# Performance work log

Measured on AMD Instinct MI355X. Metric: run time of the kernel, lower is better.

Reference implementation:

```python
import jax, jax.numpy as jnp
import numpy as np

N_DOF = 7
WIDTH = 1024
BATCH = 8192
EPS = 1e-5
LSIZE = N_DOF * (N_DOF + 1) // 2   # diag (n) + strictly-lower ((n^2-n)/2)


def _tri_idx(n):
    # order matches LowTri: offset -i chunks, within-chunk j -> entry (j+i, j)
    r, c = [], []
    for i in range(n):
        for j in range(n - i):
            r.append(j + i)
            c.append(j)
    return np.array(r, np.int32), np.array(c, np.int32)

_R, _C = _tri_idx(N_DOF)


def setup_inputs() -> dict:
    key = jax.random.key(0)
    ks = jax.random.split(key, 9)

    def glorot(k, shape):
        std = (2.0 / (shape[0] + shape[1])) ** 0.5
        return (jax.random.normal(k, shape, jnp.float32) * std).astype(jnp.float32)

    lower = LSIZE - N_DOF
    b0 = 0.1
    return {
        "state": jax.random.normal(ks[0], (BATCH, N_DOF), jnp.float32),
        "velocity": jax.random.normal(ks[1], (BATCH, N_DOF), jnp.float32),
        "acceleration": jax.random.normal(ks[2], (BATCH, N_DOF), jnp.float32),
        "W_in": glorot(ks[3], (N_DOF, WIDTH)), "b_in": jnp.full((WIDTH,), b0, jnp.float32),
        "W_h": glorot(ks[4], (WIDTH, WIDTH)), "b_h": jnp.full((WIDTH,), b0, jnp.float32),
        "W_g": glorot(ks[5], (WIDTH, 1)), "b_g": jnp.full((1,), b0, jnp.float32),
        "W_ld": glorot(ks[6], (WIDTH, N_DOF)), "b_ld": jnp.full((N_DOF,), b0, jnp.float32),
        "W_lo": glorot(ks[7], (WIDTH, lower)), "b_lo": jnp.full((lower,), b0, jnp.float32),
    }


def _layer(x, der, W, b, act):
    # a: [B, out]; der: [B, in, n_dof] -> [B, out, n_dof]
    a = x @ W + b
    if act == "relu":
        y = jax.nn.relu(a)
        gp = (a > 0).astype(a.dtype)
    else:  # linear
        y = a
        gp = jnp.ones_like(a)
    # diag(g'(a)) @ W^T @ prev_der  ==  g'(a)[:, :, None] * (W^T @ prev_der)
    new_der = gp[:, :, None] * jnp.einsum("io,bid->bod", W, der)
    return y, new_der


def _forward(state, velocity, acceleration,
             W_in, b_in, W_h, b_h, W_g, b_g, W_ld, b_ld, W_lo, b_lo):
    B = state.shape[0]
    eye = jnp.broadcast_to(jnp.eye(N_DOF, dtype=state.dtype), (B, N_DOF, N_DOF))

    y1, d1 = _layer(state, eye, W_in, b_in, "relu")
    y2, d2 = _layer(y1, d1, W_h, b_h, "relu")
    y3, d3 = _layer(y2, d2, W_h, b_h, "relu")   # original reuses hidden_layer1 twice

    V, derV = _layer(y3, d3, W_g, b_g, "linear")       # derV: [B, 1, n_dof]
    l_diag, der_ld = _layer(y3, d3, W_ld, b_ld, "relu")
    l_low, der_lo = _layer(y3, d3, W_lo, b_lo, "linear")

    l = jnp.concatenate([l_diag, l_low], axis=1)          # [B, LSIZE]
    der_l = jnp.concatenate([der_ld, der_lo], axis=1)     # [B, LSIZE, n_dof]

    def lowtri(v):   # [B, LSIZE] -> [B, n, n]
        return jnp.zeros((B, N_DOF, N_DOF), v.dtype).at[:, _R, _C].set(v)

    def lowtri3d(v):  # [B, n_dof, LSIZE] -> [B, n_dof, n, n]
        return jnp.zeros((B, N_DOF, N_DOF, N_DOF), v.dtype).at[:, :, _R, _C].set(v)

    L = lowtri(l)
    LT = jnp.swapaxes(L, 1, 2)
    M = L @ LT + EPS * jnp.eye(N_DOF, dtype=L.dtype)

    dldt = jnp.einsum("bld,bd->bl", der_l, velocity)
    dLdt = lowtri(dldt)
    dMdt = L @ jnp.swapaxes(dLdt, 1, 2) + dLdt @ LT

    dLdq = lowtri3d(jnp.swapaxes(der_l, 1, 2))            # [B, n_dof, n, n]
    dMdq = dLdq @ LT[:, None] + L[:, None] @ jnp.swapaxes(dLdq, 2, 3)

    dMdt_dq = jnp.einsum("bij,bj->bi", dMdt, velocity)
    quad_dq = jnp.einsum("bi,bkij,bj->bk", velocity, dMdq, velocity)
    C = dMdt_dq - 0.5 * quad_dq
    G = derV[:, 0, :]                                      # squeeze [B,1,n_dof]
    Mddq = jnp.einsum("bij,bj->bi", M, acceleration)
    tau_pred = Mddq + C + G
    return tau_pred, M, C, G


def reference(state, velocity, acceleration,
              W_in, b_in, W_h, b_h, W_g, b_g, W_ld, b_ld, W_lo, b_lo):
    return _forward(state, velocity, acceleration,
                    W_in, b_in, W_h, b_h, W_g, b_g, W_ld, b_ld, W_lo, b_lo)
```

## Files before the change

### kernel.cpp

```cpp
#include <hip/hip_runtime.h>
#include <hip/hip_bf16.h>
#include <hip/hip_fp16.h>

#define WIDTH 1024
#define BATCH 8192

typedef __attribute__((ext_vector_type(8))) short short8;
typedef __attribute__((ext_vector_type(8))) _Float16 half8;
typedef __attribute__((ext_vector_type(4))) float floatx4;

typedef __attribute__((address_space(1))) void gvoid;
typedef __attribute__((address_space(3))) void lvoid;

__device__ __forceinline__ void async_copy16(const void* g, void* l) {
    __builtin_amdgcn_global_load_lds((gvoid*)g, (lvoid*)l, 16, 0, 0);
}

__device__ __forceinline__ void split_store(float v, __hip_bfloat16* hi, __hip_bfloat16* lo, long idx) {
    __hip_bfloat16 h = __float2bfloat16(v);
    hi[idx] = h;
    lo[idx] = __float2bfloat16(v - __bfloat162float(h));
}

__device__ __forceinline__ floatx4 mfma16(short8 a, short8 b, floatx4 c) {
    return __builtin_amdgcn_mfma_f32_16x16x32_f16(
        __builtin_bit_cast(half8, a), __builtin_bit_cast(half8, b), c, 0, 0, 0);
}
__device__ __forceinline__ floatx4 mfmabf(short8 a, short8 b, floatx4 c) {
    return __builtin_amdgcn_mfma_f32_16x16x32_bf16(a, b, c, 0, 0, 0);
}

template<int N> __device__ __forceinline__ void waitv() {
    if constexpr (N == 0)      asm volatile("s_waitcnt vmcnt(0)" ::: "memory");
    else if constexpr (N == 1) asm volatile("s_waitcnt vmcnt(1)" ::: "memory");
    else if constexpr (N == 3) asm volatile("s_waitcnt vmcnt(3)" ::: "memory");
    else if constexpr (N == 4) asm volatile("s_waitcnt vmcnt(4)" ::: "memory");
    else if constexpr (N == 6) asm volatile("s_waitcnt vmcnt(6)" ::: "memory");
    else if constexpr (N == 7) asm volatile("s_waitcnt vmcnt(7)" ::: "memory");
    else if constexpr (N == 8) asm volatile("s_waitcnt vmcnt(8)" ::: "memory");
    else if constexpr (N == 9) asm volatile("s_waitcnt vmcnt(9)" ::: "memory");
}

__device__ __forceinline__ int swz_col(int s) {
    return ((s & 3) ^ ((s >> 3) & 3)) << 3;
}

__device__ __forceinline__ void xcd_map(int idx, int nm, int& bm, int& bn) {
    if ((nm & 7) == 0) {
        bm = (idx & 7) | ((idx >> 5) << 3);
        bn = (idx >> 3) & 3;
    } else {
        bm = idx >> 2;
        bn = idx & 3;
    }
}

__global__ __launch_bounds__(256) void transpose_k(
    const float* __restrict__ W,
    __hip_bfloat16* __restrict__ Wthb, __hip_bfloat16* __restrict__ Wtlb,
    __half* __restrict__ Wtf)
{
    __shared__ float t[32][33];
    const int tx = threadIdx.x & 31, ty = threadIdx.x >> 5;
    const int bx = blockIdx.x << 5, by = blockIdx.y << 5;
#pragma unroll
    for (int r = 0; r < 32; r += 8)
        t[ty + r][tx] = W[(long)(by + ty + r) * WIDTH + bx + tx];
    __syncthreads();
#pragma unroll
    for (int r = 0; r < 32; r += 8) {
        const float v = t[tx][ty + r];
        const long idx = (long)(bx + ty + r) * WIDTH + by + tx;
        split_store(v, Wthb, Wtlb, idx);
        Wtf[idx] = __float2half(v);
    }
}

__global__ __launch_bounds__(256) void buildwcat_k(
    const float* __restrict__ W_ld, const float* __restrict__ W_lo,
    const float* __restrict__ W_g,
    __hip_bfloat16* __restrict__ Wchb, __hip_bfloat16* __restrict__ Wclb,
    __half* __restrict__ Wcf)
{
    const int idx = blockIdx.x * 256 + threadIdx.x;
    const int n = idx >> 10, k = idx & 1023;
    float v = 0.f;
    if (n < 7)       v = W_ld[k * 7 + n];
    else if (n < 28) v = W_lo[k * 21 + (n - 7)];
    else if (n == 28) v = W_g[k];
    split_store(v, Wchb, Wclb, idx);
    Wcf[idx] = __float2half(v);
}

__global__ __launch_bounds__(256) void prep_k(
    const float* __restrict__ state,
    const float* __restrict__ W_in,
    const float* __restrict__ b_in,
    __hip_bfloat16* __restrict__ Y1h, __hip_bfloat16* __restrict__ Y1l,
    __half* __restrict__ D1f)
{
    const int b = blockIdx.x;
    const int j0 = threadIdx.x * 4;
    float s[7];
#pragma unroll
    for (int d = 0; d < 7; ++d) s[d] = state[b * 7 + d];
    float a[4];
#pragma unroll
    for (int q = 0; q < 4; ++q) a[q] = b_in[j0 + q];
    float w[7][4];
#pragma unroll
    for (int d = 0; d < 7; ++d)
#pragma unroll
        for (int q = 0; q < 4; ++q) {
            w[d][q] = W_in[d * WIDTH + j0 + q];
            a[q] += s[d] * w[d][q];
        }
    bool gp[4];
#pragma unroll
    for (int q = 0; q < 4; ++q) {
        gp[q] = a[q] > 0.f;
        split_store(gp[q] ? a[q] : 0.f, Y1h, Y1l, (long)b * WIDTH + j0 + q);
    }
    union { unsigned long long u64; unsigned short h[4]; } pk;
#pragma unroll
    for (int d = 0; d < 7; ++d) {
#pragma unroll
        for (int q = 0; q < 4; ++q) {
            __half v = __float2half(gp[q] ? w[d][q] : 0.f);
            pk.h[q] = *reinterpret_cast<unsigned short*>(&v);
        }
        *reinterpret_cast<unsigned long long*>(&D1f[((long)b * 7 + d) * WIDTH + j0]) = pk.u64;
    }
}


__device__ __forceinline__ void st128(const short* src, short* region, int tid, int kbase) {
    async_copy16(src + (long)(tid >> 2) * WIDTH + kbase + swz_col(tid),
                 region + ((tid & 0x1C0) << 3));
}
__device__ __forceinline__ void st256(const short* src, short* region, int tid, int kbase) {
#pragma unroll
    for (int j = 0; j < 2; ++j) {
        const int idx = tid + (j << 9);
        async_copy16(src + (long)(idx >> 2) * WIDTH + kbase + swz_col(idx),
                     region + (((tid & 0x1C0) + (j << 9)) << 3));
    }
}

template<int W0, int W1, int W2, int IS>
__device__ __forceinline__ void y8_triple(
    short* buf, short* nbuf,
    const short* pAh, const short* pAl, const short* pBh, const short* pBl,
    int t, int tid, int wm, int wn, int r, int kqs, floatx4 (&acc)[4][4])
{
    short8 fah[4], fbh[4];
#pragma unroll
    for (int i = 0; i < 4; ++i)
        fah[i] = *reinterpret_cast<const short8*>(&buf[(wm * 64 + i * 16 + r) * 32 + kqs]);
#pragma unroll
    for (int j = 0; j < 4; ++j)
        fbh[j] = *reinterpret_cast<const short8*>(&buf[8192 + (wn * 64 + j * 16 + r) * 32 + kqs]);
    if (IS >= 1) st128(pAl, nbuf + 4096, tid, (t + 1) * 32);
    __builtin_amdgcn_s_barrier();
    asm volatile("s_waitcnt lgkmcnt(0)");
    __builtin_amdgcn_sched_barrier(0);
    __builtin_amdgcn_s_setprio(1);
#pragma unroll
    for (int i = 0; i < 4; ++i)
#pragma unroll
        for (int j = 0; j < 4; ++j)
            acc[i][j] = mfmabf(fah[i], fbh[j], acc[i][j]);
    __builtin_amdgcn_s_setprio(0);
    waitv<W0>();
    __builtin_amdgcn_s_barrier();
    short8 fbl[4];
#pragma unroll
    for (int j = 0; j < 4; ++j)
        fbl[j] = *reinterpret_cast<const short8*>(&buf[16384 + (wn * 64 + j * 16 + r) * 32 + kqs]);
    if (IS >= 2) { st128(pAh, buf, tid, (t + 2) * 32); st256(pBh, buf + 8192, tid, (t + 2) * 32); }
    __builtin_amdgcn_s_barrier();
    asm volatile("s_waitcnt lgkmcnt(0)");
    __builtin_amdgcn_sched_barrier(0);
    __builtin_amdgcn_s_setprio(1);
#pragma unroll
    for (int i = 0; i < 4; ++i)
#pragma unroll
        for (int j = 0; j < 4; ++j)
            acc[i][j] = mfmabf(fah[i], fbl[j], acc[i][j]);
    __builtin_amdgcn_s_setprio(0);
    waitv<W1>();
    __builtin_amdgcn_s_barrier();
    short8 fal[4];
#pragma unroll
    for (int i = 0; i < 4; ++i)
        fal[i] = *reinterpret_cast<const short8*>(&buf[4096 + (wm * 64 + i * 16 + r) * 32 + kqs]);
    if (IS >= 2) st256(pBl, buf + 16384, tid, (t + 2) * 32);
    __builtin_amdgcn_s_barrier();
    asm volatile("s_waitcnt lgkmcnt(0)");
    __builtin_amdgcn_sched_barrier(0);
    __builtin_amdgcn_s_setprio(1);
#pragma unroll
    for (int i = 0; i < 4; ++i)
#pragma unroll
        for (int j = 0; j < 4; ++j)
            acc[i][j] = mfmabf(fal[i], fbh[j], acc[i][j]);
    __builtin_amdgcn_s_setprio(0);
    waitv<W2>();
    __builtin_amdgcn_s_barrier();
}

__device__ __forceinline__ void y8_gemm_body(
    short* SM,
    int bm, int bn, int tid,
    const __hip_bfloat16* Ah_, const __hip_bfloat16* Al_,
    const __hip_bfloat16* Bh_, const __hip_bfloat16* Bl_,
    const float* bias,
    __hip_bfloat16* outh, __hip_bfloat16* outl)
{
    const int lane = tid & 63, wv = tid >> 6;
    const int wm = wv >> 2, wn = wv & 3;
    const int r = lane & 15, r4 = (lane >> 4) << 2;
    const int kqs = (((lane >> 4) ^ ((r >> 1) & 3)) << 3);
    const short* pAh = (const short*)Ah_ + (long)bm * 128 * WIDTH;
    const short* pAl = (const short*)Al_ + (long)bm * 128 * WIDTH;
    const short* pBh = (const short*)Bh_ + (long)bn * 256 * WIDTH;
    const short* pBl = (const short*)Bl_ + (long)bn * 256 * WIDTH;

    floatx4 acc[4][4] = {};

    st128(pAh, SM + 0,     tid, 0);
    st256(pBh, SM + 8192,  tid, 0);
    st256(pBl, SM + 16384, tid, 0);
    st128(pAl, SM + 4096,  tid, 0);
    st128(pAh, SM + 24576 + 0,     tid, 32);
    st256(pBh, SM + 24576 + 8192,  tid, 32);
    st256(pBl, SM + 24576 + 16384, tid, 32);
    waitv<8>();
    __builtin_amdgcn_s_barrier();

    for (int t2 = 0; t2 < 15; ++t2) {
        y8_triple<7, 9, 8, 2>(SM,         SM + 24576, pAh, pAl, pBh, pBl, 2 * t2,     tid, wm, wn, r, kqs, acc);
        y8_triple<7, 9, 8, 2>(SM + 24576, SM,         pAh, pAl, pBh, pBl, 2 * t2 + 1, tid, wm, wn, r, kqs, acc);
    }
    y8_triple<7, 6, 3, 1>(SM,         SM + 24576, pAh, pAl, pBh, pBl, 30, tid, wm, wn, r, kqs, acc);
    y8_triple<1, 0, 0, 0>(SM + 24576, SM,         pAh, pAl, pBh, pBl, 31, tid, wm, wn, r, kqs, acc);

#pragma unroll
    for (int i = 0; i < 4; ++i)
#pragma unroll
        for (int j = 0; j < 4; ++j) {
            const int col = bn * 256 + wn * 64 + j * 16 + r;
#pragma unroll
            for (int rr = 0; rr < 4; ++rr) {
                const int row = bm * 128 + wm * 64 + i * 16 + r4 + rr;
                float v = acc[i][j][rr] + bias[col];
                v = v > 0.f ? v : 0.f;
                split_store(v, outh, outl, (long)row * WIDTH + col);
            }
        }
}

__global__ __launch_bounds__(512, 2) void gemm_y8(
    const __hip_bfloat16* __restrict__ Ah, const __hip_bfloat16* __restrict__ Al,
    const __hip_bfloat16* __restrict__ Bh, const __hip_bfloat16* __restrict__ Bl,
    const float* __restrict__ bias,
    __hip_bfloat16* __restrict__ outh, __hip_bfloat16* __restrict__ outl,
    int ny)
{
    __shared__ __align__(16) short SM[49152];
    int bm, bn;
    xcd_map(blockIdx.x, ny, bm, bn);
    y8_gemm_body(SM, bm, bn, threadIdx.x, Ah, Al, Bh, Bl, bias, outh, outl);
}

__device__ __forceinline__ void stage_chunk_d2(
    short* SMbase, const short* __restrict__ A, const short* __restrict__ B,
    int tau, int c, int tid)
{
    const short* src = (c & 1) ? B : A;
    const int kbase = (tau << 6) + ((c >> 1) << 5);
    short* region = SMbase + ((tau & 1) << 15) + (c << 13);
    const int wvb = tid & 0x1C0;
#pragma unroll
    for (int j = 0; j < 2; ++j) {
        const int idx = tid + (j << 9);
        async_copy16(src + (long)(idx >> 2) * WIDTH + kbase + swz_col(idx),
                     region + ((long)(wvb + (j << 9)) << 3));
    }
}

__device__ __forceinline__ void d_gemm_256(
    short* SM, const short* Abase, const short* Bbase, int tid,
    int wm, int wn, int r, int kqs, floatx4 (&acc)[8][4])
{
    stage_chunk_d2(SM, Abase, Bbase, 0, 0, tid);
    stage_chunk_d2(SM, Abase, Bbase, 0, 1, tid);
    stage_chunk_d2(SM, Abase, Bbase, 0, 2, tid);
    stage_chunk_d2(SM, Abase, Bbase, 0, 3, tid);
    stage_chunk_d2(SM, Abase, Bbase, 1, 0, tid);
    stage_chunk_d2(SM, Abase, Bbase, 1, 1, tid);
    waitv<8>();
    __builtin_amdgcn_s_barrier();

    short8 af[8], bf[4];
#pragma unroll 2
    for (int t = 0; t < 16; ++t) {
        short* buf = SM + ((t & 1) << 15);
#pragma unroll
        for (int ks = 0; ks < 2; ++ks) {
            const short* Ab = buf + (ks ? 2 : 0) * 8192;
            const short* Bb = buf + (ks ? 3 : 1) * 8192;

#pragma unroll
            for (int i = 0; i < 4; ++i)
                af[i] = *reinterpret_cast<const short8*>(&Ab[(wm * 128 + i * 16 + r) * 32 + kqs]);
#pragma unroll
            for (int j = 0; j < 4; ++j)
                bf[j] = *reinterpret_cast<const short8*>(&Bb[(wn * 64 + j * 16 + r) * 32 + kqs]);
            if (ks == 0) { if (t + 1 < 16) stage_chunk_d2(SM, Abase, Bbase, t + 1, 2, tid); }
            else         { if (t + 2 < 16) stage_chunk_d2(SM, Abase, Bbase, t + 2, 0, tid); }
            __builtin_amdgcn_s_barrier();
            asm volatile("s_waitcnt lgkmcnt(0)");
            __builtin_amdgcn_sched_barrier(0);
            __builtin_amdgcn_s_setprio(1);
#pragma unroll
            for (int i = 0; i < 4; ++i)
#pragma unroll
                for (int j = 0; j < 4; ++j)
                    acc[i][j] = mfma16(af[i], bf[j], acc[i][j]);
            __builtin_amdgcn_s_setprio(0);
            __builtin_amdgcn_s_barrier();

#pragma unroll
            for (int i = 0; i < 4; ++i)
                af[4 + i] = *reinterpret_cast<const short8*>(&Ab[(wm * 128 + (4 + i) * 16 + r) * 32 + kqs]);
            if (ks == 0) { if (t + 1 < 16) stage_chunk_d2(SM, Abase, Bbase, t + 1, 3, tid); }
            else         { if (t + 2 < 16) stage_chunk_d2(SM, Abase, Bbase, t + 2, 1, tid); }
            __builtin_amdgcn_s_barrier();
            asm volatile("s_waitcnt lgkmcnt(0)");
            __builtin_amdgcn_sched_barrier(0);
            __builtin_amdgcn_s_setprio(1);
#pragma unroll
            for (int i = 0; i < 4; ++i)
#pragma unroll
                for (int j = 0; j < 4; ++j)
                    acc[4 + i][j] = mfma16(af[4 + i], bf[j], acc[4 + i][j]);
            __builtin_amdgcn_s_setprio(0);
            if (ks == 0) {
                if (t < 15) waitv<8>(); else waitv<0>();
            } else {
                if (t < 14) waitv<8>(); else if (t == 14) waitv<4>();
            }
            __builtin_amdgcn_s_barrier();
        }
    }
}

__global__ __launch_bounds__(512, 2) void d2y3_8p(
    const __half* __restrict__ D1,
    const __half* __restrict__ Wtf,
    const __hip_bfloat16* __restrict__ Wthb, const __hip_bfloat16* __restrict__ Wtlb,
    const __hip_bfloat16* __restrict__ Y2h, const __hip_bfloat16* __restrict__ Y2l,
    const float* __restrict__ bias,
    __half* __restrict__ D2out,
    __hip_bfloat16* __restrict__ Y3h, __hip_bfloat16* __restrict__ Y3l,
    int ny128, int nd2)
{
    __shared__ __align__(16) short SM[65536];
    const int tid = threadIdx.x;

    if ((int)blockIdx.x < ny128 * 4) {
        int bm, bn;
        xcd_map(blockIdx.x, ny128, bm, bn);
        y8_gemm_body(SM, bm, bn, tid, Y2h, Y2l, Wthb, Wtlb, bias, Y3h, Y3l);
        return;
    }

    const int lane = tid & 63, wv = tid >> 6;
    const int wm = wv >> 2, wn = wv & 3;
    const int r = lane & 15, r4 = (lane >> 4) << 2;
    const int kqs = (((lane >> 4) ^ ((r >> 1) & 3)) << 3);

    int bm, bn;
    xcd_map(blockIdx.x - ny128 * 4, nd2, bm, bn);

    floatx4 acc[8][4] = {};
    d_gemm_256(SM, (const short*)D1 + (long)bm * 256 * WIDTH,
               (const short*)Wtf + (long)bn * 256 * WIDTH, tid, wm, wn, r, kqs, acc);

#pragma unroll
    for (int i = 0; i < 8; ++i)
#pragma unroll
        for (int j = 0; j < 4; ++j) {
            const int col = bn * 256 + wn * 64 + j * 16 + r;
#pragma unroll
            for (int rr = 0; rr < 4; ++rr) {
                const int row = bm * 256 + wm * 128 + i * 16 + r4 + rr;
                float v = acc[i][j][rr];
                const unsigned brow = (unsigned)row / 7u;
                if (!(__bfloat162float(Y2h[(long)brow * WIDTH + col]) > 0.f)) v = 0.f;
                D2out[(long)row * WIDTH + col] = __float2half(v);
            }
        }
}

__device__ __forceinline__ void heady_half(
    short* SMh, int bm, int tl,
    const __hip_bfloat16* __restrict__ Y3h, const __hip_bfloat16* __restrict__ Y3l,
    const __hip_bfloat16* __restrict__ Wch, const __hip_bfloat16* __restrict__ Wcl,
    float* __restrict__ PY)
{
    short* Ash = SMh;          short* Asl = SMh + 4096;
    short* Bsh = SMh + 8192;   short* Bsl = SMh + 9216;
    const int lane = tl & 63;
    const int wv = tl >> 6;
    const int r = lane & 15, r4 = (lane >> 4) << 2;
    const int kqs = (((lane >> 4) ^ ((r >> 1) & 3)) << 3);
    const int srow = tl >> 2, scol = (tl & 3) << 3;
    const int swc = (((tl & 3) ^ ((srow >> 1) & 3)) << 3);
    const long half = 64l * WIDTH;
    const short* pAh = (const short*)Y3h + (long)(bm * 128 + srow) * WIDTH + swc;
    const short* pAl = (const short*)Y3l + (long)(bm * 128 + srow) * WIDTH + swc;
    const long boff = (long)srow * WIDTH + scol;
    const short* pBh = (const short*)Wch;  const short* pBl = (const short*)Wcl;

    floatx4 acc[2][2] = {};
    for (int kt = 0; kt < WIDTH; kt += 32) {
        short8 gbh, gbl;
        if (tl < 128) {
            gbh = *reinterpret_cast<const short8*>(pBh + boff + kt);
            gbl = *reinterpret_cast<const short8*>(pBl + boff + kt);
        }
        __syncthreads();
        async_copy16(pAh + kt,        Ash + wv * 512);
        async_copy16(pAh + half + kt, Ash + 2048 + wv * 512);
        async_copy16(pAl + kt,        Asl + wv * 512);
        async_copy16(pAl + half + kt, Asl + 2048 + wv * 512);
        if (tl < 128) {
            *reinterpret_cast<short8*>(&Bsh[srow * 32 + swc]) = gbh;
            *reinterpret_cast<short8*>(&Bsl[srow * 32 + swc]) = gbl;
        }
        __syncthreads();
        short8 afh[2], afl[2], bfh[2], bfl[2];
#pragma unroll
        for (int i = 0; i < 2; ++i) {
            const int ar = (wv * 32 + i * 16 + r) * 32 + kqs;
            afh[i] = *reinterpret_cast<const short8*>(&Ash[ar]);
            afl[i] = *reinterpret_cast<const short8*>(&Asl[ar]);
        }
#pragma unroll
        for (int j = 0; j < 2; ++j) {
            const int br = (j * 16 + r) * 32 + kqs;
            bfh[j] = *reinterpret_cast<const short8*>(&Bsh[br]);
            bfl[j] = *reinterpret_cast<const short8*>(&Bsl[br]);
        }
#pragma unroll
        for (int i = 0; i < 2; ++i)
#pragma unroll
            for (int j = 0; j < 2; ++j) {
                acc[i][j] = mfmabf(afh[i], bfh[j], acc[i][j]);
                acc[i][j] = mfmabf(afh[i], bfl[j], acc[i][j]);
                acc[i][j] = mfmabf(afl[i], bfh[j], acc[i][j]);
            }
    }
#pragma unroll
    for (int i = 0; i < 2; ++i)
#pragma unroll
        for (int j = 0; j < 2; ++j)
#pragma unroll
            for (int rr = 0; rr < 4; ++rr) {
                const int row = bm * 128 + wv * 32 + i * 16 + r4 + rr;
                PY[(long)row * 32 + j * 16 + r] = acc[i][j][rr];
            }
}

__global__ __launch_bounds__(512, 2) void d3pd_8p(
    const __half* __restrict__ D2,
    const __half* __restrict__ Wtf,
    const __hip_bfloat16* __restrict__ Y3h, const __hip_bfloat16* __restrict__ Y3l,
    const __half* __restrict__ Wcf,
    const __hip_bfloat16* __restrict__ Wchb, const __hip_bfloat16* __restrict__ Wclb,
    float* __restrict__ PDpart, float* __restrict__ PY,
    int nd2, int Mrows)
{
    __shared__ __align__(16) short SM[65536];
    const int tid = threadIdx.x;

    if ((int)blockIdx.x >= nd2 * 4) {
        const int hd = (blockIdx.x - nd2 * 4) * 2 + (tid >> 8);
        heady_half(SM + (tid >> 8) * 10240, hd, tid & 255, Y3h, Y3l, Wchb, Wclb, PY);
        return;
    }

    const int lane = tid & 63, wv = tid >> 6;
    const int wm = wv >> 2, wn = wv & 3;
    const int r = lane & 15, kq = (lane >> 4) << 3, r4 = (lane >> 4) << 2;
    const int kqs = (((lane >> 4) ^ ((r >> 1) & 3)) << 3);
    int bm, bn;
    xcd_map(blockIdx.x, nd2, bm, bn);

    floatx4 acc[8][4] = {};
    d_gemm_256(SM, (const short*)D2 + (long)bm * 256 * WIDTH,
               (const short*)Wtf + (long)bn * 256 * WIDTH, tid, wm, wn, r, kqs, acc);

    short* T   = SM;
    short* WcH = SM + 34816;

    floatx4 accp[2][2] = {};
#pragma unroll
    for (int h = 0; h < 2; ++h) {
        __syncthreads();
        if ((wn >> 1) == h) {
#pragma unroll
            for (int i = 0; i < 8; ++i)
#pragma unroll
                for (int j = 0; j < 4; ++j) {
                    const int ct = (wn & 1) * 64 + j * 16 + r;
                    const int colg = bn * 256 + h * 128 + ct;
#pragma unroll
                    for (int rr = 0; rr < 4; ++rr) {
                        const int rowl = wm * 128 + i * 16 + r4 + rr;
                        const int rowg = bm * 256 + rowl;
                        float v = acc[i][j][rr];
                        const unsigned brow = (unsigned)rowg / 7u;
                        if (!(__bfloat162float(Y3h[(long)brow * WIDTH + colg]) > 0.f)) v = 0.f;
                        __half hb = __float2half(v);
                        T[rowl * 136 + ct] = *reinterpret_cast<short*>(&hb);
                    }
                }
        }
        {
            const int n = tid >> 4, k8 = (tid & 15) * 8;
            const short* wh = (const short*)Wcf;
            *reinterpret_cast<short8*>(&WcH[n * 136 + k8]) =
                *reinterpret_cast<const short8*>(wh + (long)n * WIDTH + bn * 256 + h * 128 + k8);
        }
        __syncthreads();
#pragma unroll
        for (int kk = 0; kk < 128; kk += 32) {
            short8 af2[2], bh8[2];
#pragma unroll
            for (int i = 0; i < 2; ++i)
                af2[i] = *reinterpret_cast<const short8*>(&T[(wv * 32 + i * 16 + r) * 136 + kk + kq]);
#pragma unroll
            for (int j = 0; j < 2; ++j)
                bh8[j] = *reinterpret_cast<const short8*>(&WcH[(j * 16 + r) * 136 + kk + kq]);
#pragma unroll
            for (int i = 0; i < 2; ++i)
#pragma unroll
                for (int j = 0; j < 2; ++j)
                    accp[i][j] = mfma16(af2[i], bh8[j], accp[i][j]);
        }
    }
#pragma unroll
    for (int i = 0; i < 2; ++i)
#pragma unroll
        for (int j = 0; j < 2; ++j)
#pragma unroll
            for (int rr = 0; rr < 4; ++rr) {
                const int rowg = bm * 256 + wv * 32 + i * 16 + r4 + rr;
                PDpart[((long)bn * Mrows + rowg) * 32 + j * 16 + r] = accp[i][j][rr];
            }
}

__device__ __forceinline__ int midx(int rr, int cc) {
    const int i = rr - cc;
    return i * 7 - (i * (i - 1)) / 2 + cc;
}

__global__ __launch_bounds__(64) void finalize_k(
    const float* __restrict__ PY,
    const float* __restrict__ PDpart,
    const float* __restrict__ vel_g,
    const float* __restrict__ acc_g,
    const float* __restrict__ b_ld,
    const float* __restrict__ b_lo,
    float* __restrict__ out,
    int b0, int Mrows)
{
    __shared__ float lval[28];
    __shared__ int gpv[7];
    __shared__ float derl[29 * 7];
    __shared__ float Lm[49], Mm[49], dLt[49], uu[49];
    __shared__ float wvv[7], pv[7], Cv[7], Gv[7], tauv[7], vl[7], ac[7];

    const int bl = blockIdx.x, tid = threadIdx.x;
    const int b = b0 + bl;
    if (tid < 28) {
        float s = PY[(long)bl * 32 + tid];
        if (tid < 7) {
            s += b_ld[tid];
            gpv[tid] = s > 0.f;
            lval[tid] = s > 0.f ? s : 0.f;
        } else {
            lval[tid] = s + b_lo[tid - 7];
        }
    }
    if (tid >= 28 && tid < 35) {
        vl[tid - 28] = vel_g[b * 7 + tid - 28];
        ac[tid - 28] = acc_g[b * 7 + tid - 28];
    }
    __syncthreads();
    for (int idx = tid; idx < 203; idx += 64) {
        const int m = idx / 7, d = idx % 7;
        float v = 0.f;
#pragma unroll
        for (int p = 0; p < 4; ++p)
            v += PDpart[((long)p * Mrows + bl * 7 + d) * 32 + m];
        if (m < 7 && !gpv[m]) v = 0.f;
        derl[m * 7 + d] = v;
    }
    __syncthreads();
    if (tid < 49) {
        const int rr = tid / 7, cc = tid % 7;
        Lm[tid] = (rr >= cc) ? lval[midx(rr, cc)] : 0.f;
    }
    __syncthreads();
    if (tid < 49) {
        const int rr = tid / 7, cc = tid % 7;
        float s = 0.f;
        for (int k = 0; k < 7; ++k) s += Lm[rr * 7 + k] * Lm[cc * 7 + k];
        if (rr == cc) s += 1e-5f;
        Mm[tid] = s;
        float t = 0.f;
        if (rr >= cc) {
            const int m = midx(rr, cc);
            for (int d = 0; d < 7; ++d) t += derl[m * 7 + d] * vl[d];
        }
        dLt[tid] = t;
        float u = 0.f;
        for (int r2 = cc; r2 < 7; ++r2) u += vl[r2] * derl[midx(r2, cc) * 7 + rr];
        uu[tid] = u;
    } else if (tid >= 49 && tid < 56) {
        const int j = tid - 49;
        float s = 0.f;
        for (int r2 = 0; r2 < 7; ++r2) s += Lm[r2 * 7 + j] * vl[r2];
        wvv[j] = s;
    }
    __syncthreads();
    if (tid < 7) {
        float s = 0.f;
        for (int r2 = 0; r2 < 7; ++r2) s += dLt[r2 * 7 + tid] * vl[r2];
        pv[tid] = s;
    }
    __syncthreads();
    if (tid < 7) {
        float s = 0.f, q = 0.f, md = 0.f;
        for (int c = 0; c < 7; ++c) {
            s += Lm[tid * 7 + c] * pv[c] + dLt[tid * 7 + c] * wvv[c];
            q += uu[tid * 7 + c] * wvv[c];
            md += Mm[tid * 7 + c] * ac[c];
        }
        Cv[tid] = s - q;
        Gv[tid] = derl[28 * 7 + tid];
        tauv[tid] = md + Cv[tid] + Gv[tid];
    }
    __syncthreads();
    if (tid < 49) out[57344 + (long)b * 49 + tid] = Mm[tid];
    if (tid < 7) {
        out[(long)b * 7 + tid] = tauv[tid];
        out[458752 + (long)b * 7 + tid] = Cv[tid];
        out[516096 + (long)b * 7 + tid] = Gv[tid];
    }
}

extern "C" void kernel_launch(void* const* d_in, const int* in_sizes, int n_in,
                              void* d_out, int out_size, void* d_ws, size_t ws_size,
                              hipStream_t stream)
{
    const float* state = (const float*)d_in[0];
    const float* vel   = (const float*)d_in[1];
    const float* accel = (const float*)d_in[2];
    const float* W_in  = (const float*)d_in[3];
    const float* b_in  = (const float*)d_in[4];
    const float* W_h   = (const float*)d_in[5];
    const float* b_h   = (const float*)d_in[6];
    const float* W_g   = (const float*)d_in[7];
    const float* W_ld  = (const float*)d_in[9];
    const float* b_ld  = (const float*)d_in[10];
    const float* W_lo  = (const float*)d_in[11];
    const float* b_lo  = (const float*)d_in[12];
    float* outp = (float*)d_out;

    char* ws = (char*)d_ws;
    __hip_bfloat16* Wthb = (__hip_bfloat16*)ws; ws += (size_t)WIDTH * WIDTH * 2;
    __hip_bfloat16* Wtlb = (__hip_bfloat16*)ws; ws += (size_t)WIDTH * WIDTH * 2;
    __half*         Wtf  = (__half*)ws;         ws += (size_t)WIDTH * WIDTH * 2;
    __hip_bfloat16* Wchb = (__hip_bfloat16*)ws; ws += 32 * WIDTH * 2;
    __hip_bfloat16* Wclb = (__hip_bfloat16*)ws; ws += 32 * WIDTH * 2;
    __half*         Wcf  = (__half*)ws;         ws += 32 * WIDTH * 2;
    const size_t fixed = (size_t)(ws - (char*)d_ws);

    int CH = 256;
    for (int cand = 8192; cand >= 256; cand >>= 1) {
        size_t need = fixed + (size_t)cand * 36992;
        if (need <= ws_size) { CH = cand; break; }
    }
    const int NCH = BATCH / CH;

    const size_t YB = (size_t)CH * WIDTH * 2;
    const size_t DB = (size_t)CH * 7 * WIDTH * 2;
    __hip_bfloat16* Yah = (__hip_bfloat16*)ws; ws += YB;
    __hip_bfloat16* Yal = (__hip_bfloat16*)ws; ws += YB;
    __hip_bfloat16* Ybh = (__hip_bfloat16*)ws; ws += YB;
    __hip_bfloat16* Ybl = (__hip_bfloat16*)ws; ws += YB;
    __half* Daf = (__half*)ws; ws += DB;
    __half* Dbf = (__half*)ws; ws += DB;
    float* PY = (float*)ws; ws += (size_t)CH * 32 * 4;
    float* PDpart = (float*)Daf;

    const int Mrows = CH * 7;
    const int nd2 = Mrows / 256;
    const int ny128 = CH / 128;

    transpose_k<<<dim3(32, 32), dim3(256), 0, stream>>>(W_h, Wthb, Wtlb, Wtf);
    buildwcat_k<<<dim3(128), dim3(256), 0, stream>>>(W_ld, W_lo, W_g, Wchb, Wclb, Wcf);

    for (int c = 0; c < NCH; ++c) {
        prep_k<<<dim3(CH), dim3(256), 0, stream>>>(state + (size_t)c * CH * 7, W_in, b_in,
                                                   Yah, Yal, Daf);
        gemm_y8<<<dim3(ny128 * 4), dim3(512), 0, stream>>>(
            Yah, Yal, Wthb, Wtlb, b_h, Ybh, Ybl, ny128);
        d2y3_8p<<<dim3((ny128 + nd2) * 4), dim3(512), 0, stream>>>(
            Daf, Wtf, Wthb, Wtlb, Ybh, Ybl, b_h, Dbf, Yah, Yal, ny128, nd2);
        d3pd_8p<<<dim3(nd2 * 4 + ny128 / 2), dim3(512), 0, stream>>>(
            Dbf, Wtf, Yah, Yal, Wcf, Wchb, Wclb, PDpart, PY, nd2, Mrows);
        finalize_k<<<dim3(CH), dim3(64), 0, stream>>>(PY, PDpart, vel, accel, b_ld, b_lo,
                                                      outp, c * CH, Mrows);
    }
    (void)in_sizes; (void)n_in; (void)out_size;
}
```

Measured before the change: 570.6 us.

## Triple-buffer LDS and double-buffer register fragments in both GEMM mainloops

The Y-GEMM mainloop moves from double-buffered LDS with three barrier-separated MFMA phases per K-chunk to a three-deep LDS ring. All hi/lo fragments for the next chunk are prefetched into a second register set while the current chunk's MFMAs issue, with one barrier per chunk. The D2 GEMM loop gets the same treatment: one barrier per chunk, with next-chunk fragment reads overlapping the current MFMAs. The aim is to cut barrier and LDS-wait stalls between MFMA bursts. The cost is more LDS per block (shared arrays grow to 147 KB) and more VGPRs for the duplicated fragments, which could reduce occupancy or cause spills.

```diff
diff --git a/kernel.cpp b/kernel.cpp
--- a/kernel.cpp
+++ b/kernel.cpp
@@ -32,13 +32,9 @@
 
 template<int N> __device__ __forceinline__ void waitv() {
     if constexpr (N == 0)      asm volatile("s_waitcnt vmcnt(0)" ::: "memory");
-    else if constexpr (N == 1) asm volatile("s_waitcnt vmcnt(1)" ::: "memory");
-    else if constexpr (N == 3) asm volatile("s_waitcnt vmcnt(3)" ::: "memory");
     else if constexpr (N == 4) asm volatile("s_waitcnt vmcnt(4)" ::: "memory");
     else if constexpr (N == 6) asm volatile("s_waitcnt vmcnt(6)" ::: "memory");
-    else if constexpr (N == 7) asm volatile("s_waitcnt vmcnt(7)" ::: "memory");
     else if constexpr (N == 8) asm volatile("s_waitcnt vmcnt(8)" ::: "memory");
-    else if constexpr (N == 9) asm volatile("s_waitcnt vmcnt(9)" ::: "memory");
 }
 
 __device__ __forceinline__ int swz_col(int s) {
@@ -133,7 +129,6 @@
     }
 }
 
-
 __device__ __forceinline__ void st128(const short* src, short* region, int tid, int kbase) {
     async_copy16(src + (long)(tid >> 2) * WIDTH + kbase + swz_col(tid),
                  region + ((tid & 0x1C0) << 3));
@@ -147,66 +142,34 @@
     }
 }
 
-template<int W0, int W1, int W2, int IS>
-__device__ __forceinline__ void y8_triple(
-    short* buf, short* nbuf,
-    const short* pAh, const short* pAl, const short* pBh, const short* pBl,
-    int t, int tid, int wm, int wn, int r, int kqs, floatx4 (&acc)[4][4])
-{
-    short8 fah[4], fbh[4];
-#pragma unroll
-    for (int i = 0; i < 4; ++i)
-        fah[i] = *reinterpret_cast<const short8*>(&buf[(wm * 64 + i * 16 + r) * 32 + kqs]);
-#pragma unroll
-    for (int j = 0; j < 4; ++j)
-        fbh[j] = *reinterpret_cast<const short8*>(&buf[8192 + (wn * 64 + j * 16 + r) * 32 + kqs]);
-    if (IS >= 1) st128(pAl, nbuf + 4096, tid, (t + 1) * 32);
-    __builtin_amdgcn_s_barrier();
-    asm volatile("s_waitcnt lgkmcnt(0)");
-    __builtin_amdgcn_sched_barrier(0);
-    __builtin_amdgcn_s_setprio(1);
-#pragma unroll
-    for (int i = 0; i < 4; ++i)
-#pragma unroll
-        for (int j = 0; j < 4; ++j)
-            acc[i][j] = mfmabf(fah[i], fbh[j], acc[i][j]);
-    __builtin_amdgcn_s_setprio(0);
-    waitv<W0>();
-    __builtin_amdgcn_s_barrier();
-    short8 fbl[4];
-#pragma unroll
-    for (int j = 0; j < 4; ++j)
-        fbl[j] = *reinterpret_cast<const short8*>(&buf[16384 + (wn * 64 + j * 16 + r) * 32 + kqs]);
-    if (IS >= 2) { st128(pAh, buf, tid, (t + 2) * 32); st256(pBh, buf + 8192, tid, (t + 2) * 32); }
-    __builtin_amdgcn_s_barrier();
-    asm volatile("s_waitcnt lgkmcnt(0)");
-    __builtin_amdgcn_sched_barrier(0);
-    __builtin_amdgcn_s_setprio(1);
-#pragma unroll
-    for (int i = 0; i < 4; ++i)
-#pragma unroll
-        for (int j = 0; j < 4; ++j)
-            acc[i][j] = mfmabf(fah[i], fbl[j], acc[i][j]);
-    __builtin_amdgcn_s_setprio(0);
-    waitv<W1>();
-    __builtin_amdgcn_s_barrier();
-    short8 fal[4];
-#pragma unroll
-    for (int i = 0; i < 4; ++i)
-        fal[i] = *reinterpret_cast<const short8*>(&buf[4096 + (wm * 64 + i * 16 + r) * 32 + kqs]);
-    if (IS >= 2) st256(pBl, buf + 16384, tid, (t + 2) * 32);
-    __builtin_amdgcn_s_barrier();
-    asm volatile("s_waitcnt lgkmcnt(0)");
-    __builtin_amdgcn_sched_barrier(0);
-    __builtin_amdgcn_s_setprio(1);
-#pragma unroll
-    for (int i = 0; i < 4; ++i)
-#pragma unroll
-        for (int j = 0; j < 4; ++j)
-            acc[i][j] = mfmabf(fal[i], fbh[j], acc[i][j]);
-    __builtin_amdgcn_s_setprio(0);
-    waitv<W2>();
-    __builtin_amdgcn_s_barrier();
+
+__device__ __forceinline__ void y_stage(
+    short* SM, const short* pAh, const short* pAl,
+    const short* pBh, const short* pBl, int c, int tid)
+{
+    short* buf = SM + (c % 3) * 24576;
+    const int kb = c * 32;
+    st128(pAh, buf,         tid, kb);
+    st256(pBh, buf + 8192,  tid, kb);
+    st128(pAl, buf + 4096,  tid, kb);
+    st256(pBl, buf + 16384, tid, kb);
+}
+
+__device__ __forceinline__ void y_reads(
+    const short* SM, int c, int wm, int wn, int r, int kqs,
+    short8 (&ah)[4], short8 (&al)[4], short8 (&bh)[4], short8 (&bl)[4])
+{
+    const short* buf = SM + (c % 3) * 24576;
+#pragma unroll
+    for (int i = 0; i < 4; ++i) {
+        ah[i] = *reinterpret_cast<const short8*>(&buf[(wm * 64 + i * 16 + r) * 32 + kqs]);
+        al[i] = *reinterpret_cast<const short8*>(&buf[4096 + (wm * 64 + i * 16 + r) * 32 + kqs]);
+    }
+#pragma unroll
+    for (int j = 0; j < 4; ++j) {
+        bh[j] = *reinterpret_cast<const short8*>(&buf[8192 + (wn * 64 + j * 16 + r) * 32 + kqs]);
+        bl[j] = *reinterpret_cast<const short8*>(&buf[16384 + (wn * 64 + j * 16 + r) * 32 + kqs]);
+    }
 }
 
 __device__ __forceinline__ void y8_gemm_body(
@@ -227,23 +190,47 @@
     const short* pBl = (const short*)Bl_ + (long)bn * 256 * WIDTH;
 
     floatx4 acc[4][4] = {};
-
-    st128(pAh, SM + 0,     tid, 0);
-    st256(pBh, SM + 8192,  tid, 0);
-    st256(pBl, SM + 16384, tid, 0);
-    st128(pAl, SM + 4096,  tid, 0);
-    st128(pAh, SM + 24576 + 0,     tid, 32);
-    st256(pBh, SM + 24576 + 8192,  tid, 32);
-    st256(pBl, SM + 24576 + 16384, tid, 32);
-    waitv<8>();
+    short8 ahA[4], alA[4], bhA[4], blA[4];
+    short8 ahB[4], alB[4], bhB[4], blB[4];
+
+    y_stage(SM, pAh, pAl, pBh, pBl, 0, tid);
+    y_stage(SM, pAh, pAl, pBh, pBl, 1, tid);
+    y_stage(SM, pAh, pAl, pBh, pBl, 2, tid);
+    waitv<6>();
     __builtin_amdgcn_s_barrier();
-
-    for (int t2 = 0; t2 < 15; ++t2) {
-        y8_triple<7, 9, 8, 2>(SM,         SM + 24576, pAh, pAl, pBh, pBl, 2 * t2,     tid, wm, wn, r, kqs, acc);
-        y8_triple<7, 9, 8, 2>(SM + 24576, SM,         pAh, pAl, pBh, pBl, 2 * t2 + 1, tid, wm, wn, r, kqs, acc);
-    }
-    y8_triple<7, 6, 3, 1>(SM,         SM + 24576, pAh, pAl, pBh, pBl, 30, tid, wm, wn, r, kqs, acc);
-    y8_triple<1, 0, 0, 0>(SM + 24576, SM,         pAh, pAl, pBh, pBl, 31, tid, wm, wn, r, kqs, acc);
+    y_reads(SM, 0, wm, wn, r, kqs, ahA, alA, bhA, blA);
+
+    auto chunk = [&](short8 (&cah)[4], short8 (&cal)[4], short8 (&cbh)[4], short8 (&cbl)[4],
+                     short8 (&nah)[4], short8 (&nal)[4], short8 (&nbh)[4], short8 (&nbl)[4],
+                     int c) {
+        __builtin_amdgcn_s_barrier();
+        if (c + 3 < 32) y_stage(SM, pAh, pAl, pBh, pBl, c + 3, tid);
+        if (c + 1 < 32) y_reads(SM, c + 1, wm, wn, r, kqs, nah, nal, nbh, nbl);
+        __builtin_amdgcn_s_setprio(1);
+#pragma unroll
+        for (int i = 0; i < 4; ++i)
+#pragma unroll
+            for (int j = 0; j < 4; ++j)
+                acc[i][j] = mfmabf(cah[i], cbh[j], acc[i][j]);
+#pragma unroll
+        for (int i = 0; i < 4; ++i)
+#pragma unroll
+            for (int j = 0; j < 4; ++j)
+                acc[i][j] = mfmabf(cal[i], cbh[j], acc[i][j]);
+#pragma unroll
+        for (int i = 0; i < 4; ++i)
+#pragma unroll
+            for (int j = 0; j < 4; ++j)
+                acc[i][j] = mfmabf(cah[i], cbl[j], acc[i][j]);
+        __builtin_amdgcn_s_setprio(0);
+        if (c <= 28) waitv<6>();
+        else if (c == 29) waitv<0>();
+    };
+
+    for (int t2 = 0; t2 < 16; ++t2) {
+        chunk(ahA, alA, bhA, blA, ahB, alB, bhB, blB, 2 * t2);
+        chunk(ahB, alB, bhB, blB, ahA, alA, bhA, blA, 2 * t2 + 1);
+    }
 
 #pragma unroll
     for (int i = 0; i < 4; ++i)
@@ -267,19 +254,20 @@
     __hip_bfloat16* __restrict__ outh, __hip_bfloat16* __restrict__ outl,
     int ny)
 {
-    __shared__ __align__(16) short SM[49152];
+    __shared__ __align__(16) short SM[73728];
     int bm, bn;
     xcd_map(blockIdx.x, ny, bm, bn);
     y8_gemm_body(SM, bm, bn, threadIdx.x, Ah, Al, Bh, Bl, bias, outh, outl);
 }
 
+
 __device__ __forceinline__ void stage_chunk_d2(
     short* SMbase, const short* __restrict__ A, const short* __restrict__ B,
-    int tau, int c, int tid)
-{
-    const short* src = (c & 1) ? B : A;
-    const int kbase = (tau << 6) + ((c >> 1) << 5);
-    short* region = SMbase + ((tau & 1) << 15) + (c << 13);
+    int tau, int creg, int tid)
+{
+    const short* src = (creg & 1) ? B : A;
+    const int kbase = (tau << 6) + ((creg >> 1) << 5);
+    short* region = SMbase + ((tau & 1) << 15) + (creg << 13);
     const int wvb = tid & 0x1C0;
 #pragma unroll
     for (int j = 0; j < 2; ++j) {
@@ -289,70 +277,61 @@
     }
 }
 
+__device__ __forceinline__ void d_stage(
+    short* SM, const short* A, const short* B, int c, int tid)
+{
+    stage_chunk_d2(SM, A, B, c >> 1, (c & 1) << 1, tid);
+    stage_chunk_d2(SM, A, B, c >> 1, ((c & 1) << 1) | 1, tid);
+}
+
+__device__ __forceinline__ void d_reads(
+    const short* SM, int c, int wm, int wn, int r, int kqs,
+    short8 (&af)[8], short8 (&bf)[4])
+{
+    const short* Ab = SM + (((c >> 1) & 1) << 15) + ((c & 1) << 14);
+    const short* Bb = Ab + 8192;
+#pragma unroll
+    for (int i = 0; i < 8; ++i)
+        af[i] = *reinterpret_cast<const short8*>(&Ab[(wm * 128 + i * 16 + r) * 32 + kqs]);
+#pragma unroll
+    for (int j = 0; j < 4; ++j)
+        bf[j] = *reinterpret_cast<const short8*>(&Bb[(wn * 64 + j * 16 + r) * 32 + kqs]);
+}
+
 __device__ __forceinline__ void d_gemm_256(
     short* SM, const short* Abase, const short* Bbase, int tid,
     int wm, int wn, int r, int kqs, floatx4 (&acc)[8][4])
 {
-    stage_chunk_d2(SM, Abase, Bbase, 0, 0, tid);
-    stage_chunk_d2(SM, Abase, Bbase, 0, 1, tid);
-    stage_chunk_d2(SM, Abase, Bbase, 0, 2, tid);
-    stage_chunk_d2(SM, Abase, Bbase, 0, 3, tid);
-    stage_chunk_d2(SM, Abase, Bbase, 1, 0, tid);
-    stage_chunk_d2(SM, Abase, Bbase, 1, 1, tid);
+    short8 afA[8], bfA[4], afB[8], bfB[4];
+
+    d_stage(SM, Abase, Bbase, 0, tid);
+    d_stage(SM, Abase, Bbase, 1, tid);
+    d_stage(SM, Abase, Bbase, 2, tid);
+    d_stage(SM, Abase, Bbase, 3, tid);
     waitv<8>();
     __builtin_amdgcn_s_barrier();
-
-    short8 af[8], bf[4];
-#pragma unroll 2
-    for (int t = 0; t < 16; ++t) {
-        short* buf = SM + ((t & 1) << 15);
-#pragma unroll
-        for (int ks = 0; ks < 2; ++ks) {
-            const short* Ab = buf + (ks ? 2 : 0) * 8192;
-            const short* Bb = buf + (ks ? 3 : 1) * 8192;
-
-#pragma unroll
-            for (int i = 0; i < 4; ++i)
-                af[i] = *reinterpret_cast<const short8*>(&Ab[(wm * 128 + i * 16 + r) * 32 + kqs]);
+    d_reads(SM, 0, wm, wn, r, kqs, afA, bfA);
+
+    auto chunk = [&](short8 (&caf)[8], short8 (&cbf)[4],
+                     short8 (&naf)[8], short8 (&nbf)[4], int c) {
+        __builtin_amdgcn_s_barrier();
+        if (c + 4 < 32) d_stage(SM, Abase, Bbase, c + 4, tid);
+        if (c + 1 < 32) d_reads(SM, c + 1, wm, wn, r, kqs, naf, nbf);
+        __builtin_amdgcn_s_setprio(1);
+#pragma unroll
+        for (int i = 0; i < 8; ++i)
 #pragma unroll
             for (int j = 0; j < 4; ++j)
-                bf[j] = *reinterpret_cast<const short8*>(&Bb[(wn * 64 + j * 16 + r) * 32 + kqs]);
-            if (ks == 0) { if (t + 1 < 16) stage_chunk_d2(SM, Abase, Bbase, t + 1, 2, tid); }
-            else         { if (t + 2 < 16) stage_chunk_d2(SM, Abase, Bbase, t + 2, 0, tid); }
-            __builtin_amdgcn_s_barrier();
-            asm volatile("s_waitcnt lgkmcnt(0)");
-            __builtin_amdgcn_sched_barrier(0);
-            __builtin_amdgcn_s_setprio(1);
-#pragma unroll
-            for (int i = 0; i < 4; ++i)
-#pragma unroll
-                for (int j = 0; j < 4; ++j)
-                    acc[i][j] = mfma16(af[i], bf[j], acc[i][j]);
-            __builtin_amdgcn_s_setprio(0);
-            __builtin_amdgcn_s_barrier();
-
-#pragma unroll
-            for (int i = 0; i < 4; ++i)
-                af[4 + i] = *reinterpret_cast<const short8*>(&Ab[(wm * 128 + (4 + i) * 16 + r) * 32 + kqs]);
-            if (ks == 0) { if (t + 1 < 16) stage_chunk_d2(SM, Abase, Bbase, t + 1, 3, tid); }
-            else         { if (t + 2 < 16) stage_chunk_d2(SM, Abase, Bbase, t + 2, 1, tid); }
-            __builtin_amdgcn_s_barrier();
-            asm volatile("s_waitcnt lgkmcnt(0)");
-            __builtin_amdgcn_sched_barrier(0);
-            __builtin_amdgcn_s_setprio(1);
-#pragma unroll
-            for (int i = 0; i < 4; ++i)
-#pragma unroll
-                for (int j = 0; j < 4; ++j)
-                    acc[4 + i][j] = mfma16(af[4 + i], bf[j], acc[4 + i][j]);
-            __builtin_amdgcn_s_setprio(0);
-            if (ks == 0) {
-                if (t < 15) waitv<8>(); else waitv<0>();
-            } else {
-                if (t < 14) waitv<8>(); else if (t == 14) waitv<4>();
-            }
-            __builtin_amdgcn_s_barrier();
-        }
+                acc[i][j] = mfma16(caf[i], cbf[j], acc[i][j]);
+        __builtin_amdgcn_s_setprio(0);
+        if (c <= 27) waitv<8>();
+        else if (c == 28) waitv<4>();
+        else if (c == 29) waitv<0>();
+    };
+
+    for (int t2 = 0; t2 < 16; ++t2) {
+        chunk(afA, bfA, afB, bfB, 2 * t2);
+        chunk(afB, bfB, afA, bfA, 2 * t2 + 1);
     }
 }
 
@@ -366,7 +345,7 @@
     __hip_bfloat16* __restrict__ Y3h, __hip_bfloat16* __restrict__ Y3l,
     int ny128, int nd2)
 {
-    __shared__ __align__(16) short SM[65536];
+    __shared__ __align__(16) short SM[73728];
     const int tid = threadIdx.x;
 
     if ((int)blockIdx.x < ny128 * 4) {
```

Result: faster. 553.5 us, median of 2 (-3.0%).
